# Optimization experiments

Hardware: AMD Instinct MI355X
Metric: run time of the kernel (lower is better)

Reference implementation:

```python
import jax, jax.numpy as jnp
import numpy as np

NODE_FEAT = 200  # F.interpolate size in run_all_node
TOPN = 2         # StitchModel.topn


def _node_feats(img, mask, flow, n_inst, max_pix):
    """Vectorized run_all_node: per-instance gather, linear interp to NODE_FEAT,
    3x3 sign histogram of flow[:2], mean of flow[2]. mask holds labels 1..n_inst;
    max_pix is a static upper bound on pixels per instance."""
    flat = mask.reshape(-1) - 1                       # labels 0..N-1
    order = jnp.argsort(flat)                         # stable sort by label
    counts = jax.ops.segment_sum(jnp.ones_like(flat), flat, num_segments=n_inst)
    starts = jnp.concatenate([jnp.zeros((1,), counts.dtype), jnp.cumsum(counts)[:-1]])
    j = jnp.arange(max_pix)
    pos = starts[:, None] + jnp.minimum(j[None, :], counts[:, None] - 1)
    idx = order[pos]                                  # [N, max_pix] padded pixel indices
    valid = j[None, :] < counts[:, None]              # [N, max_pix]
    iv = img.reshape(-1)[idx]                         # instance intensity profiles
    fx = flow[0].reshape(-1)[idx]
    fy = flow[1].reshape(-1)[idx]
    fz = flow[2].reshape(-1)[idx]
    cf = counts.astype(img.dtype)
    zflow = jnp.where(valid, fz, 0).sum(1) / cf       # flows[-1][m].mean()

    def interp(v, L):                                 # torch linear interp, align_corners=False
        Lf = L.astype(img.dtype)
        p = jnp.clip((jnp.arange(NODE_FEAT, dtype=img.dtype) + 0.5) * (Lf / NODE_FEAT) - 0.5,
                     0.0, Lf - 1.0)
        i0 = jnp.floor(p).astype(jnp.int32)
        i1 = jnp.minimum(i0 + 1, L - 1)
        w = p - i0.astype(img.dtype)
        return v[i0] * (1 - w) + v[i1] * w

    nodes = jax.vmap(interp)(iv, counts)              # [N, 200]
    # hist_flow_vector: bins ordered (x:<0,==0,>0) x (y:<0,==0,>0) -> 3*cx+cy
    cx = jnp.where(fx < 0, 0, jnp.where(fx == 0, 1, 2))
    cy = jnp.where(fy < 0, 0, jnp.where(fy == 0, 1, 2))
    bins = cx * 3 + cy
    oh = (bins[..., None] == jnp.arange(9)) & valid[..., None]
    hist = oh.sum(1).astype(img.dtype)                # [N, 9]
    return jnp.concatenate([nodes, hist], -1), zflow


def setup_inputs() -> dict:
    H = W = 2048
    N = 4096
    pix = (H * W) // N
    key = jax.random.key(0)
    ks = jax.random.split(key, 8)

    def make_mask(k):
        labels = (jnp.arange(H * W, dtype=jnp.int32) // pix) + 1   # labels 1..N
        perm = jax.random.permutation(k, H * W)
        return labels[perm].reshape(H, W)

    def make_bbox(k):
        u = jax.random.uniform(k, (N, 4), jnp.float32)
        centers = u[:, :2] * H
        sizes = u[:, 2:] * 49.0 + 1.0                               # nonzero w/h (asserted)
        return jnp.concatenate([centers, sizes], -1)

    return {
        "img1": jax.random.normal(ks[0], (H, W), jnp.float32),
        "img2": jax.random.normal(ks[1], (H, W), jnp.float32),
        "flow1": jax.random.normal(ks[2], (3, H, W), jnp.float32),
        "flow2": jax.random.normal(ks[3], (3, H, W), jnp.float32),
        "bbox1": make_bbox(ks[4]),
        "bbox2": make_bbox(ks[5]),
        "mask1": make_mask(ks[6]),
        "mask2": make_mask(ks[7]),
    }


def reference(img1, img2, flow1, flow2, bbox1, bbox2, mask1, mask2):
    N1, N2 = bbox1.shape[0], bbox2.shape[0]
    max1 = mask1.size // N1   # static bound on pixels/instance (equal-partition masks)
    max2 = mask2.size // N2
    node1, zf1 = _node_feats(img1, mask1, flow1, N1, max1)
    node2, zf2 = _node_feats(img2, mask2, flow2, N2, max2)
    x = jnp.concatenate([node1, node2], 0)            # [(N1+N2), 209]
    # build_one_graph_low_ram: per row, TOPN smallest center distances
    d = jnp.sqrt(((bbox1[:, None, :2] - bbox2[None, :, :2]) ** 2).sum(-1))  # [N1,N2]
    _, nbr = jax.lax.top_k(-d, TOPN)                  # smallest-first, like argsort[:topn]
    src = jnp.repeat(jnp.arange(N1), TOPN)            # [N1*TOPN]
    dst = nbr.reshape(-1)
    edge_index = jnp.stack([src, dst + N1])           # [2, N1*TOPN]
    edge_attr = jnp.stack([
        zf1[src], zf2[dst],
        bbox1[src, 0] - bbox2[dst, 0],
        bbox1[src, 1] - bbox2[dst, 1],
        bbox1[src, 2] / bbox2[dst, 2],
        bbox1[src, 3] / bbox2[dst, 3],
    ], -1)                                            # [N1*TOPN, 6]
    return x, edge_index, edge_attr
```

## Files before the change

kernel.cpp:

```cpp
#include <hip/hip_runtime.h>
#include <math.h>

#pragma clang fp contract(off)

#define HW      (2048*2048)
#define NI      4096
#define MAXPIX  1024
#define NF      200
#define FEAT    209
#define NE      (NI*2)
#define XSIZE   ((2*NI)*FEAT)
#define EIOFF   XSIZE
#define EAOFF   (EIOFF + 2*NE)

#define S       8192
#define CHK     (HW/S)
#define TOTCHK  (2*CHK)
#define NBPI    256
#define LPB     16
#define NBG     (2*NBPI)
#define REC     (2*HW)
#define BTOT    (LPB*MAXPIX)
#define NWS     16
#define NXCD    8
#define ZROWS   512

template<int NB>
__device__ __forceinline__ unsigned long long match_bits(int v) {
    unsigned long long m = ~0ull;
    #pragma unroll
    for (int bit = 0; bit < NB; ++bit) {
        unsigned long long bb = __ballot((v >> bit) & 1);
        m &= ((v >> bit) & 1) ? bb : ~bb;
    }
    return m;
}

__global__ void __launch_bounds__(1024) count_zf_kernel(const int* __restrict__ mask1,
        const int* __restrict__ mask2, const float* __restrict__ flow1,
        const float* __restrict__ flow2, unsigned* __restrict__ cntA,
        float* __restrict__ zfpart) {
    __shared__ unsigned cnt[16][NBPI];
    __shared__ float zfp[NI];
    int t = threadIdx.x, w = t >> 6, lane = t & 63;
    for (int j = t; j < 16*NBPI; j += 1024) ((unsigned*)cnt)[j] = 0u;
    for (int j = t; j < NI; j += 1024) zfp[j] = 0.f;
    __syncthreads();
    int c0 = blockIdx.x * 2;
    int img = c0 / CHK;
    int c = c0 + (w >> 3);
    const int4*   mask  = (const int4*)(img ? mask2 : mask1);
    const float4* flowz = (const float4*)((img ? flow2 : flow1) + 2L*HW);
    long base4 = (long)(c - img*CHK) * (S/4) + (long)(w & 7) * (S/32);
    #pragma unroll
    for (int it = 0; it < S/32; it += 64) {
        int4   l4 = mask[base4 + it + lane];
        float4 fz = flowz[base4 + it + lane];
        atomicAdd(&cnt[w][(l4.x-1) >> 4], 1u);
        atomicAdd(&cnt[w][(l4.y-1) >> 4], 1u);
        atomicAdd(&cnt[w][(l4.z-1) >> 4], 1u);
        atomicAdd(&cnt[w][(l4.w-1) >> 4], 1u);
        atomicAdd(&zfp[l4.x-1], fz.x);
        atomicAdd(&zfp[l4.y-1], fz.y);
        atomicAdd(&zfp[l4.z-1], fz.z);
        atomicAdd(&zfp[l4.w-1], fz.w);
    }
    __syncthreads();
    if (t < 2*NBPI) {
        int cc = c0 + (t >> 8), b = t & (NBPI - 1);
        int r0 = (t >> 8) * 8;
        unsigned s = 0;
        #pragma unroll
        for (int q = 0; q < 8; ++q) s += cnt[r0 + q][b];
        cntA[(long)cc * NBPI + b] = s;
    }
    float* zdst = zfpart + (long)blockIdx.x * NI;
    for (int j = t; j < NI; j += 1024) zdst[j] = zfp[j];
}

#define SCB 16
__global__ void __launch_bounds__(1024) scan_kernel(unsigned* __restrict__ cntA) {
    __shared__ int wsum[16][SCB];
    __shared__ int pbase[SCB];
    int t = threadIdx.x, w = t >> 6, lane = t & 63;
    int b = blockIdx.x;
    int img = b >> 4;
    int b0 = (b & 15) * SCB;
    int bk = lane & 15, r4 = lane >> 4;
    if (t < SCB) pbase[t] = 0;
    __syncthreads();
    for (int pass = 0; pass < 8; ++pass) {
        int row = pass*64 + w*4 + r4;
        long idx = ((long)img*CHK + row)*NBPI + b0 + bk;
        unsigned e = cntA[idx];
        int incl = (int)e, o;
        o = __shfl_up(incl, 16); if (lane >= 16) incl += o;
        o = __shfl_up(incl, 32); if (lane >= 32) incl += o;
        if (lane >= 48) wsum[w][bk] = incl;
        __syncthreads();
        int add = pbase[bk];
        #pragma unroll
        for (int q = 0; q < 16; ++q) if (q < w) add += wsum[q][bk];
        cntA[idx] = (unsigned)(incl + add - (int)e);
        __syncthreads();
        if (t < SCB) {
            int s = 0;
            #pragma unroll
            for (int q = 0; q < 16; ++q) s += wsum[q][t];
            pbase[t] += s;
        }
        __syncthreads();
    }
}

__global__ void __launch_bounds__(1024, 8) sort_kernel(
        const float* __restrict__ img1, const float* __restrict__ img2,
        const float* __restrict__ flow1, const float* __restrict__ flow2,
        const int* __restrict__ mask1, const int* __restrict__ mask2,
        const unsigned* __restrict__ cntA,
        float* __restrict__ riv, unsigned char* __restrict__ rmeta) {
    __shared__ float ivs[S];
    __shared__ unsigned short smeta[S];
    __shared__ unsigned short cw[NWS][NBPI];
    __shared__ int gofs[NBPI];
    int* wsum = (int*)smeta;
    int t = threadIdx.x, w = t >> 6, lane = t & 63;
    int bid = blockIdx.x;
    int c = (bid & (NXCD-1)) * (TOTCHK/NXCD) + (bid >> 3);
    int img = c / CHK;
    const int*   mask  = img ? mask2  : mask1;
    const float* image = img ? img2   : img1;
    const float* flow  = img ? flow2  : flow1;
    long base = (long)(c - img*CHK) * S;
    unsigned pre = 0;
    if (t < NBPI) pre = cntA[(long)c * NBPI + t];
    for (int j = t; j < NWS*NBPI; j += 1024) ((unsigned short*)cw)[j] = 0;
    {
        const int4*   mk = (const int4*)mask;
        const float4* iv = (const float4*)image;
        const float4* fx = (const float4*)flow;
        const float4* fy = (const float4*)(flow + HW);
        long i0 = (base >> 2) + (long)w*128 + lane;
        long i1 = i0 + 64;
        int4   m0 = mk[i0], m1 = mk[i1];
        float4 v0 = iv[i0], v1 = iv[i1];
        float4 x0 = fx[i0], x1 = fx[i1];
        float4 y0 = fy[i0], y1 = fy[i1];
        int p0 = (w<<9) + (lane<<2);
        ushort4 s0, s1;
        s0.x = (unsigned short)((m0.x-1) | (((x0.x<0.f?0:(x0.x==0.f?1:2))*3 + (y0.x<0.f?0:(y0.x==0.f?1:2))) << 12));
        s0.y = (unsigned short)((m0.y-1) | (((x0.y<0.f?0:(x0.y==0.f?1:2))*3 + (y0.y<0.f?0:(y0.y==0.f?1:2))) << 12));
        s0.z = (unsigned short)((m0.z-1) | (((x0.z<0.f?0:(x0.z==0.f?1:2))*3 + (y0.z<0.f?0:(y0.z==0.f?1:2))) << 12));
        s0.w = (unsigned short)((m0.w-1) | (((x0.w<0.f?0:(x0.w==0.f?1:2))*3 + (y0.w<0.f?0:(y0.w==0.f?1:2))) << 12));
        s1.x = (unsigned short)((m1.x-1) | (((x1.x<0.f?0:(x1.x==0.f?1:2))*3 + (y1.x<0.f?0:(y1.x==0.f?1:2))) << 12));
        s1.y = (unsigned short)((m1.y-1) | (((x1.y<0.f?0:(x1.y==0.f?1:2))*3 + (y1.y<0.f?0:(y1.y==0.f?1:2))) << 12));
        s1.z = (unsigned short)((m1.z-1) | (((x1.z<0.f?0:(x1.z==0.f?1:2))*3 + (y1.z<0.f?0:(y1.z==0.f?1:2))) << 12));
        s1.w = (unsigned short)((m1.w-1) | (((x1.w<0.f?0:(x1.w==0.f?1:2))*3 + (y1.w<0.f?0:(y1.w==0.f?1:2))) << 12));
        *(float4*)&ivs[p0]         = v0;
        *(float4*)&ivs[p0 + 256]   = v1;
        *(ushort4*)&smeta[p0]       = s0;
        *(ushort4*)&smeta[p0 + 256] = s1;
    }
    __syncthreads();
    int   pk[8];
    float piv[8];
    unsigned long long ltmask = (1ull << lane) - 1ull;
    #pragma unroll
    for (int it = 0; it < 8; ++it) {
        int p = (w<<9) + (it<<6) + lane;
        float ivx = ivs[p];
        int mt = (int)smeta[p];
        int bkt = (mt & 4095) >> 4;
        unsigned long long m = match_bits<8>(bkt);
        int cb = __popcll(m & ltmask);
        int ct = __popcll(m);
        piv[it] = ivx;
        pk[it] = (mt & 0xFFFF) | (cb << 16) | (ct << 22);
        if (cb == 0) cw[w][bkt] += (unsigned short)ct;
    }
    __syncthreads();
    int tot = 0, incl = 0;
    if (t < NBPI) {
        #pragma unroll
        for (int q = 0; q < NWS; ++q) tot += cw[q][t];
        incl = tot;
        #pragma unroll
        for (int off = 1; off < 64; off <<= 1) {
            int o = __shfl_up(incl, off);
            if (lane >= off) incl += o;
        }
        if (lane == 63) wsum[w] = incl;
    }
    __syncthreads();
    if (t < NBPI) {
        int add = 0;
        for (int q = 0; q < w; ++q) add += wsum[q];
        int excl = incl + add - tot;
        int run = excl;
        #pragma unroll
        for (int q = 0; q < NWS; ++q) {
            int cq = cw[q][t];
            cw[q][t] = (unsigned short)run;
            run += cq;
        }
        gofs[t] = (img*NBPI + t) * BTOT + (int)pre - excl;
    }
    __syncthreads();
    #pragma unroll
    for (int it = 0; it < 8; ++it) {
        int pkv = pk[it];
        int l = pkv & 4095, bin = (pkv >> 12) & 15;
        int cb = (pkv >> 16) & 63, ct = (pkv >> 22) & 127;
        int bkt = l >> 4;
        int r0 = (int)cw[w][bkt];
        int dst = r0 + cb;
        if (cb == ct - 1) cw[w][bkt] = (unsigned short)(r0 + ct);
        ivs[dst] = piv[it];
        smeta[dst] = (unsigned short)((bkt << 8) | (bin << 4) | (l & 15));
    }
    __syncthreads();
    for (int j = t; j < S; j += 1024) {
        int ms = (int)smeta[j];
        int b = ms >> 8;
        int g = gofs[b] + j;
        riv[g]   = ivs[j];
        rmeta[g] = (unsigned char)(ms & 0xFF);
    }
}

__global__ void __launch_bounds__(1024) stageB_kernel(
        const float* __restrict__ riv, const unsigned char* __restrict__ rmeta,
        const float* __restrict__ zfpart, float* __restrict__ out,
        float* __restrict__ zfm) {
    __shared__ float acc[LPB * NF];
    __shared__ float s_tw[MAXPIX];
    __shared__ int   s_tk[MAXPIX];
    __shared__ int   hist[LPB * 9];
    __shared__ int   qc[16][LPB];
    __shared__ int   cur[16][LPB];
    __shared__ float red[16][64];
    int t = threadIdx.x, w = t >> 6, lane = t & 63;
    int b = blockIdx.x;
    if (b >= NBG) {
        int b2 = b - NBG;
        int img = b2 >> 6;
        int l0  = (b2 & 63) * 64;
        const float* p = zfpart + ((long)img*(ZROWS/2) + w)*NI + l0 + lane;
        float s = 0.f;
        #pragma unroll
        for (int r = 0; r < ZROWS/2; r += 16) s += p[(long)r*NI];
        red[w][lane] = s;
        __syncthreads();
        if (t < 64) {
            float sum = 0.f;
            #pragma unroll
            for (int g = 0; g < 16; ++g) sum += red[g][t];
            zfm[img*NI + l0 + t] = sum * (1.0f/(float)MAXPIX);
        }
        return;
    }
    for (int j = t; j < LPB*NF; j += 1024) acc[j] = 0.f;
    if (t < MAXPIX) s_tk[t] = -1;
    if (t < LPB*9) hist[t] = 0;
    if (t < 16*LPB) ((int*)qc)[t] = 0;
    __syncthreads();
    if (t < NF) {
        const float Lf = (float)MAXPIX;
        float p = ((float)t + 0.5f) * (Lf / (float)NF) - 0.5f;
        p = fminf(fmaxf(p, 0.0f), Lf - 1.0f);
        int i0 = (int)floorf(p);
        int i1 = min(i0 + 1, MAXPIX - 1);
        float wg = p - (float)i0;
        s_tk[i0] = t; s_tw[i0] = 1.0f - wg;
        s_tk[i1] = t; s_tw[i1] = wg;
    }
    long base = (long)b * BTOT;
    const int qsz = BTOT / 16;
    int qbeg = w * qsz;
    unsigned long long ltmask = (1ull << lane) - 1ull;
    {
        const uchar4* rm4 = (const uchar4*)(rmeta + base + qbeg);
        #pragma unroll
        for (int it = 0; it < 4; ++it) {
            uchar4 m = rm4[it*64 + lane];
            int l0 = m.x & 15, l1 = m.y & 15, l2 = m.z & 15, l3 = m.w & 15;
            unsigned long long mm;
            mm = match_bits<4>(l0); if ((mm & ltmask) == 0) qc[w][l0] += __popcll(mm);
            mm = match_bits<4>(l1); if ((mm & ltmask) == 0) qc[w][l1] += __popcll(mm);
            mm = match_bits<4>(l2); if ((mm & ltmask) == 0) qc[w][l2] += __popcll(mm);
            mm = match_bits<4>(l3); if ((mm & ltmask) == 0) qc[w][l3] += __popcll(mm);
        }
    }
    __syncthreads();
    if (t < LPB) {
        int s = 0;
        #pragma unroll
        for (int q = 0; q < 16; ++q) { cur[q][t] = s; s += qc[q][t]; }
    }
    __syncthreads();
    #pragma unroll
    for (int it = 0; it < 16; ++it) {
        int i = qbeg + it*64 + lane;
        int meta = (int)rmeta[base + i];
        float iv = riv[base + i];
        int ll = meta & 15;
        unsigned long long mll = match_bits<4>(ll);
        int cb = __popcll(mll & ltmask);
        int ct = __popcll(mll);
        int r0 = cur[w][ll];
        int rank = r0 + cb;
        if (cb == ct - 1) cur[w][ll] = r0 + ct;
        atomicAdd(&hist[ll*9 + (meta >> 4)], 1);
        int k = s_tk[rank];
        if (k >= 0) atomicAdd(&acc[ll*NF + k], iv * s_tw[rank]);
    }
    __syncthreads();
    for (int j = t; j < LPB*FEAT; j += 1024) {
        int r = j / FEAT, k = j - r*FEAT;
        float v = (k < NF) ? acc[r*NF + k] : (float)hist[r*9 + (k - NF)];
        out[(long)b * LPB * FEAT + j] = v;
    }
}

__device__ __forceinline__ bool better(float d, int j, float d2, int j2) {
    return d < d2 || (d == d2 && j < j2);
}

__global__ void __launch_bounds__(256) edge_kernel(const float* __restrict__ bbox1,
                                                   const float* __restrict__ bbox2,
                                                   const float* __restrict__ zfm,
                                                   float* __restrict__ out) {
    __shared__ float sbx[NI], sby[NI];
    int wave = threadIdx.x >> 6, lane = threadIdx.x & 63;
    for (int r = threadIdx.x; r < NI; r += 256) {
        float4 b = ((const float4*)bbox2)[r];
        sbx[r] = b.x; sby[r] = b.y;
    }
    __syncthreads();
    int i = blockIdx.x * 4 + wave;
    float c1x = bbox1[i*4 + 0], c1y = bbox1[i*4 + 1];
    float d0 = INFINITY; int j0 = 0x7fffffff;
    float d1 = INFINITY; int j1 = 0x7fffffff;
    for (int t = 0; t < NI; t += 64) {
        int j = t + lane;
        float dx = c1x - sbx[j];
        float dy = c1y - sby[j];
        float dsq = dx*dx + dy*dy;
        float d = (float)sqrt((double)dsq);
        if (better(d, j, d0, j0)) { d1 = d0; j1 = j0; d0 = d; j0 = j; }
        else if (better(d, j, d1, j1)) { d1 = d; j1 = j; }
    }
    for (int off = 32; off; off >>= 1) {
        float od0 = __shfl_down(d0, off); int oj0 = __shfl_down(j0, off);
        float od1 = __shfl_down(d1, off); int oj1 = __shfl_down(j1, off);
        if (better(od0, oj0, d0, j0)) {
            if (better(d0, j0, od1, oj1)) { d1 = d0; j1 = j0; }
            else                          { d1 = od1; j1 = oj1; }
            d0 = od0; j0 = oj0;
        } else if (better(od0, oj0, d1, j1)) { d1 = od0; j1 = oj0; }
    }
    if (lane == 0) {
        float z1 = zfm[i];
        int js[2] = { j0, j1 };
        for (int t = 0; t < 2; ++t) {
            int e = i*2 + t, j = js[t];
            out[EIOFF + e]      = (float)i;
            out[EIOFF + NE + e] = (float)(j + NI);
            float* ea = out + EAOFF + (long)e * 6;
            ea[0] = z1;
            ea[1] = zfm[NI + j];
            ea[2] = c1x - bbox2[j*4 + 0];
            ea[3] = c1y - bbox2[j*4 + 1];
            ea[4] = bbox1[i*4 + 2] / bbox2[j*4 + 2];
            ea[5] = bbox1[i*4 + 3] / bbox2[j*4 + 3];
        }
    }
}

extern "C" void kernel_launch(void* const* d_in, const int* in_sizes, int n_in,
                              void* d_out, int out_size, void* d_ws, size_t ws_size,
                              hipStream_t stream) {
    const float* img1  = (const float*)d_in[0];
    const float* img2  = (const float*)d_in[1];
    const float* flow1 = (const float*)d_in[2];
    const float* flow2 = (const float*)d_in[3];
    const float* bbox1 = (const float*)d_in[4];
    const float* bbox2 = (const float*)d_in[5];
    const int*   mask1 = (const int*)d_in[6];
    const int*   mask2 = (const int*)d_in[7];
    float* out = (float*)d_out;

    char* ws = (char*)d_ws;
    size_t off = 0;
    unsigned* cntA   = (unsigned*)(ws + off); off += (size_t)TOTCHK * NBPI * 4;
    float*    riv    = (float*)(ws + off);    off += (size_t)REC * 4;
    float*    zfpart = (float*)(ws + off);    off += (size_t)ZROWS * NI * 4;
    float*    zfm    = (float*)(ws + off);    off += 2 * NI * 4;
    unsigned char* rmeta = (unsigned char*)(ws + off); off += (size_t)REC;

    hipLaunchKernelGGL(count_zf_kernel, dim3(TOTCHK/2), dim3(1024), 0, stream,
                       mask1, mask2, flow1, flow2, cntA, zfpart);
    hipLaunchKernelGGL(scan_kernel, dim3(32), dim3(1024), 0, stream, cntA);
    hipLaunchKernelGGL(sort_kernel, dim3(TOTCHK), dim3(1024), 0, stream,
                       img1, img2, flow1, flow2, mask1, mask2, cntA, riv, rmeta);
    hipLaunchKernelGGL(stageB_kernel, dim3(NBG + 128), dim3(1024), 0, stream,
                       riv, rmeta, zfpart, out, zfm);
    hipLaunchKernelGGL(edge_kernel, dim3(NI/4), dim3(256), 0, stream,
                       bbox1, bbox2, zfm, out);
}
```

Measured before the change: 302.6 us.

## Move zflow reduction into scan kernel and fuse edge kernel into stageB

The zflow partial-sum reduction moves from stageB into the scan kernel as 128 extra blocks, so zfm is ready earlier. The nearest-neighbour edge computation is then folded into the stageB launch as 256 extra blocks of 16 waves each. This removes one kernel launch and lets the edge work overlap with the stageB histogram blocks instead of running after them. The cost is extra shared memory in stageB (32 KB for the bbox2 centers), which may lower occupancy of the main stageB blocks.

```diff
diff --git a/kernel.cpp b/kernel.cpp
--- a/kernel.cpp
+++ b/kernel.cpp
@@ -79,37 +79,57 @@
 }
 
 #define SCB 16
-__global__ void __launch_bounds__(1024) scan_kernel(unsigned* __restrict__ cntA) {
+__global__ void __launch_bounds__(1024) scan_zf_kernel(unsigned* __restrict__ cntA,
+        const float* __restrict__ zfpart, float* __restrict__ zfm) {
     __shared__ int wsum[16][SCB];
     __shared__ int pbase[SCB];
+    __shared__ float red[16][64];
     int t = threadIdx.x, w = t >> 6, lane = t & 63;
     int b = blockIdx.x;
-    int img = b >> 4;
-    int b0 = (b & 15) * SCB;
-    int bk = lane & 15, r4 = lane >> 4;
-    if (t < SCB) pbase[t] = 0;
-    __syncthreads();
-    for (int pass = 0; pass < 8; ++pass) {
-        int row = pass*64 + w*4 + r4;
-        long idx = ((long)img*CHK + row)*NBPI + b0 + bk;
-        unsigned e = cntA[idx];
-        int incl = (int)e, o;
-        o = __shfl_up(incl, 16); if (lane >= 16) incl += o;
-        o = __shfl_up(incl, 32); if (lane >= 32) incl += o;
-        if (lane >= 48) wsum[w][bk] = incl;
+    if (b < 32) {
+        int img = b >> 4;
+        int b0 = (b & 15) * SCB;
+        int bk = lane & 15, r4 = lane >> 4;
+        if (t < SCB) pbase[t] = 0;
         __syncthreads();
-        int add = pbase[bk];
-        #pragma unroll
-        for (int q = 0; q < 16; ++q) if (q < w) add += wsum[q][bk];
-        cntA[idx] = (unsigned)(incl + add - (int)e);
+        for (int pass = 0; pass < 8; ++pass) {
+            int row = pass*64 + w*4 + r4;
+            long idx = ((long)img*CHK + row)*NBPI + b0 + bk;
+            unsigned e = cntA[idx];
+            int incl = (int)e, o;
+            o = __shfl_up(incl, 16); if (lane >= 16) incl += o;
+            o = __shfl_up(incl, 32); if (lane >= 32) incl += o;
+            if (lane >= 48) wsum[w][bk] = incl;
+            __syncthreads();
+            int add = pbase[bk];
+            #pragma unroll
+            for (int q = 0; q < 16; ++q) if (q < w) add += wsum[q][bk];
+            cntA[idx] = (unsigned)(incl + add - (int)e);
+            __syncthreads();
+            if (t < SCB) {
+                int s = 0;
+                #pragma unroll
+                for (int q = 0; q < 16; ++q) s += wsum[q][t];
+                pbase[t] += s;
+            }
+            __syncthreads();
+        }
+    } else {
+        int b2 = b - 32;
+        int img = b2 >> 6;
+        int l0  = (b2 & 63) * 64;
+        const float* p = zfpart + ((long)img*(ZROWS/2) + w)*NI + l0 + lane;
+        float s = 0.f;
+        #pragma unroll
+        for (int r = 0; r < ZROWS/2; r += 16) s += p[(long)r*NI];
+        red[w][lane] = s;
         __syncthreads();
-        if (t < SCB) {
-            int s = 0;
+        if (t < 64) {
+            float sum = 0.f;
             #pragma unroll
-            for (int q = 0; q < 16; ++q) s += wsum[q][t];
-            pbase[t] += s;
-        }
-        __syncthreads();
+            for (int g = 0; g < 16; ++g) sum += red[g][t];
+            zfm[img*NI + l0 + t] = sum * (1.0f/(float)MAXPIX);
+        }
     }
 }
 
@@ -228,34 +248,66 @@
     }
 }
 
-__global__ void __launch_bounds__(1024) stageB_kernel(
+__device__ __forceinline__ bool better(float d, int j, float d2, int j2) {
+    return d < d2 || (d == d2 && j < j2);
+}
+
+__global__ void __launch_bounds__(1024) stageB_edge_kernel(
         const float* __restrict__ riv, const unsigned char* __restrict__ rmeta,
-        const float* __restrict__ zfpart, float* __restrict__ out,
-        float* __restrict__ zfm) {
+        const float* __restrict__ bbox1, const float* __restrict__ bbox2,
+        const float* __restrict__ zfm, float* __restrict__ out) {
     __shared__ float acc[LPB * NF];
     __shared__ float s_tw[MAXPIX];
     __shared__ int   s_tk[MAXPIX];
     __shared__ int   hist[LPB * 9];
     __shared__ int   qc[16][LPB];
     __shared__ int   cur[16][LPB];
-    __shared__ float red[16][64];
+    __shared__ float sbx[NI], sby[NI];
     int t = threadIdx.x, w = t >> 6, lane = t & 63;
     int b = blockIdx.x;
     if (b >= NBG) {
-        int b2 = b - NBG;
-        int img = b2 >> 6;
-        int l0  = (b2 & 63) * 64;
-        const float* p = zfpart + ((long)img*(ZROWS/2) + w)*NI + l0 + lane;
-        float s = 0.f;
-        #pragma unroll
-        for (int r = 0; r < ZROWS/2; r += 16) s += p[(long)r*NI];
-        red[w][lane] = s;
+        int i = (b - NBG) * 16 + w;
+        for (int r = t; r < NI; r += 1024) {
+            float4 bb = ((const float4*)bbox2)[r];
+            sbx[r] = bb.x; sby[r] = bb.y;
+        }
         __syncthreads();
-        if (t < 64) {
-            float sum = 0.f;
-            #pragma unroll
-            for (int g = 0; g < 16; ++g) sum += red[g][t];
-            zfm[img*NI + l0 + t] = sum * (1.0f/(float)MAXPIX);
+        float c1x = bbox1[i*4 + 0], c1y = bbox1[i*4 + 1];
+        float d0 = INFINITY; int j0 = 0x7fffffff;
+        float d1 = INFINITY; int j1 = 0x7fffffff;
+        for (int tt = 0; tt < NI; tt += 64) {
+            int j = tt + lane;
+            float dx = c1x - sbx[j];
+            float dy = c1y - sby[j];
+            float dsq = dx*dx + dy*dy;
+            float d = (float)sqrt((double)dsq);
+            if (better(d, j, d0, j0)) { d1 = d0; j1 = j0; d0 = d; j0 = j; }
+            else if (better(d, j, d1, j1)) { d1 = d; j1 = j; }
+        }
+        for (int off = 32; off; off >>= 1) {
+            float od0 = __shfl_down(d0, off); int oj0 = __shfl_down(j0, off);
+            float od1 = __shfl_down(d1, off); int oj1 = __shfl_down(j1, off);
+            if (better(od0, oj0, d0, j0)) {
+                if (better(d0, j0, od1, oj1)) { d1 = d0; j1 = j0; }
+                else                          { d1 = od1; j1 = oj1; }
+                d0 = od0; j0 = oj0;
+            } else if (better(od0, oj0, d1, j1)) { d1 = od0; j1 = oj0; }
+        }
+        if (lane == 0) {
+            float z1 = zfm[i];
+            int js[2] = { j0, j1 };
+            for (int tt = 0; tt < 2; ++tt) {
+                int e = i*2 + tt, j = js[tt];
+                out[EIOFF + e]      = (float)i;
+                out[EIOFF + NE + e] = (float)(j + NI);
+                float* ea = out + EAOFF + (long)e * 6;
+                ea[0] = z1;
+                ea[1] = zfm[NI + j];
+                ea[2] = c1x - bbox2[j*4 + 0];
+                ea[3] = c1y - bbox2[j*4 + 1];
+                ea[4] = bbox1[i*4 + 2] / bbox2[j*4 + 2];
+                ea[5] = bbox1[i*4 + 3] / bbox2[j*4 + 3];
+            }
         }
         return;
     }
@@ -322,61 +374,6 @@
     }
 }
 
-__device__ __forceinline__ bool better(float d, int j, float d2, int j2) {
-    return d < d2 || (d == d2 && j < j2);
-}
-
-__global__ void __launch_bounds__(256) edge_kernel(const float* __restrict__ bbox1,
-                                                   const float* __restrict__ bbox2,
-                                                   const float* __restrict__ zfm,
-                                                   float* __restrict__ out) {
-    __shared__ float sbx[NI], sby[NI];
-    int wave = threadIdx.x >> 6, lane = threadIdx.x & 63;
-    for (int r = threadIdx.x; r < NI; r += 256) {
-        float4 b = ((const float4*)bbox2)[r];
-        sbx[r] = b.x; sby[r] = b.y;
-    }
-    __syncthreads();
-    int i = blockIdx.x * 4 + wave;
-    float c1x = bbox1[i*4 + 0], c1y = bbox1[i*4 + 1];
-    float d0 = INFINITY; int j0 = 0x7fffffff;
-    float d1 = INFINITY; int j1 = 0x7fffffff;
-    for (int t = 0; t < NI; t += 64) {
-        int j = t + lane;
-        float dx = c1x - sbx[j];
-        float dy = c1y - sby[j];
-        float dsq = dx*dx + dy*dy;
-        float d = (float)sqrt((double)dsq);
-        if (better(d, j, d0, j0)) { d1 = d0; j1 = j0; d0 = d; j0 = j; }
-        else if (better(d, j, d1, j1)) { d1 = d; j1 = j; }
-    }
-    for (int off = 32; off; off >>= 1) {
-        float od0 = __shfl_down(d0, off); int oj0 = __shfl_down(j0, off);
-        float od1 = __shfl_down(d1, off); int oj1 = __shfl_down(j1, off);
-        if (better(od0, oj0, d0, j0)) {
-            if (better(d0, j0, od1, oj1)) { d1 = d0; j1 = j0; }
-            else                          { d1 = od1; j1 = oj1; }
-            d0 = od0; j0 = oj0;
-        } else if (better(od0, oj0, d1, j1)) { d1 = od0; j1 = oj0; }
-    }
-    if (lane == 0) {
-        float z1 = zfm[i];
-        int js[2] = { j0, j1 };
-        for (int t = 0; t < 2; ++t) {
-            int e = i*2 + t, j = js[t];
-            out[EIOFF + e]      = (float)i;
-            out[EIOFF + NE + e] = (float)(j + NI);
-            float* ea = out + EAOFF + (long)e * 6;
-            ea[0] = z1;
-            ea[1] = zfm[NI + j];
-            ea[2] = c1x - bbox2[j*4 + 0];
-            ea[3] = c1y - bbox2[j*4 + 1];
-            ea[4] = bbox1[i*4 + 2] / bbox2[j*4 + 2];
-            ea[5] = bbox1[i*4 + 3] / bbox2[j*4 + 3];
-        }
-    }
-}
-
 extern "C" void kernel_launch(void* const* d_in, const int* in_sizes, int n_in,
                               void* d_out, int out_size, void* d_ws, size_t ws_size,
                               hipStream_t stream) {
@@ -400,11 +397,10 @@
 
     hipLaunchKernelGGL(count_zf_kernel, dim3(TOTCHK/2), dim3(1024), 0, stream,
                        mask1, mask2, flow1, flow2, cntA, zfpart);
-    hipLaunchKernelGGL(scan_kernel, dim3(32), dim3(1024), 0, stream, cntA);
+    hipLaunchKernelGGL(scan_zf_kernel, dim3(32 + 128), dim3(1024), 0, stream,
+                       cntA, zfpart, zfm);
     hipLaunchKernelGGL(sort_kernel, dim3(TOTCHK), dim3(1024), 0, stream,
                        img1, img2, flow1, flow2, mask1, mask2, cntA, riv, rmeta);
-    hipLaunchKernelGGL(stageB_kernel, dim3(NBG + 128), dim3(1024), 0, stream,
-                       riv, rmeta, zfpart, out, zfm);
-    hipLaunchKernelGGL(edge_kernel, dim3(NI/4), dim3(256), 0, stream,
-                       bbox1, bbox2, zfm, out);
-}
+    hipLaunchKernelGGL(stageB_edge_kernel, dim3(NBG + 256), dim3(1024), 0, stream,
+                       riv, rmeta, bbox1, bbox2, zfm, out);
+}
```

After: 296.9 us. Within noise of the previous version (-1.9%).
